# Performance work log

Hardware: AMD Instinct MI355X
Metric: run time of the kernel (lower is better)

## Reference

```python
import jax, jax.numpy as jnp
import numpy as np

B, S, D = 32, 512, 1024  # batch, seq_len, input_dim == output_dim


def setup_inputs() -> dict:
    key = jax.random.key(0)
    ks = jax.random.split(key, 13)
    std = 0.05  # tf.random_normal_initializer default stddev
    w = lambda k, shp: (jax.random.normal(k, shp, dtype=jnp.float32) * std)
    inp = {"seq_input_vec": jax.random.normal(ks[0], (B, S, D), dtype=jnp.float32)}
    names = ["Ui", "Wi", "Uf", "Wf", "Uo", "Wo", "Ug", "Wg"]
    for i, n in enumerate(names):
        inp[n] = w(ks[1 + i], (D, D))
    for n in ["bi", "bf", "bo", "bg"]:
        inp[n] = jnp.zeros((D,), dtype=jnp.float32)
    return inp


def reference(seq_input_vec, Ui, Wi, bi, Uf, Wf, bf, Uo, Wo, bo, Ug, Wg, bg):
    # seq_input_vec: [B, S, D]. Fuse the 4 input projections into one GEMM
    # over the whole sequence (mathematically identical to per-step matmuls).
    U = jnp.concatenate([Ui, Uf, Uo, Ug], axis=1)          # [D, 4D]
    W = jnp.concatenate([Wi, Wf, Wo, Wg], axis=1)          # [D, 4D]
    b = jnp.concatenate([bi, bf, bo, bg], axis=0)          # [4D]
    x_proj = jnp.einsum('bsd,de->sbe', seq_input_vec, U) + b  # [S, B, 4D]

    d = seq_input_vec.shape[-1]
    h0 = jnp.zeros((seq_input_vec.shape[0], d), dtype=seq_input_vec.dtype)
    c0 = jnp.zeros_like(h0)

    def step(carry, xp):
        c_prev, h_prev = carry
        z = xp + h_prev @ W                                 # [B, 4D]
        zi, zf, zo, zg = jnp.split(z, 4, axis=-1)
        i_t = jax.nn.sigmoid(zi)
        f_t = jax.nn.sigmoid(zf)
        o_t = jax.nn.sigmoid(zo)
        g_t = jnp.tanh(zg)
        # NOTE: original (nonstandard) math applies sigmoid to the cell update
        c_t = jax.nn.sigmoid(f_t * c_prev + i_t * g_t)
        h_t = jnp.tanh(c_t) * o_t
        return (c_t, h_t), h_t

    _, hs = jax.lax.scan(step, (c0, h0), x_proj)            # hs: [S, B, D]
    return jnp.transpose(hs, (1, 0, 2))                     # [B, S, D]
```

## Files before the change

### kernel.cpp

```cpp
#include <hip/hip_runtime.h>

typedef unsigned int u32;
typedef unsigned short u16;
typedef unsigned long long u64;
typedef __attribute__((ext_vector_type(8))) short short8;
typedef __attribute__((ext_vector_type(4))) float f32x4;
typedef __attribute__((ext_vector_type(4))) u32 u32x4;
typedef __attribute__((ext_vector_type(2))) u32 u32x2;

#define SEQ 512
#define BATCH 32
#define DIM 1024
#define NB 128

#define OFF_XT    0ull
#define OFF_UBT   33554432ull
#define OFF_WG2   41943040ull
#define OFF_XPROJ 50331648ull
#define OFF_BIAS  184680448ull
#define OFF_SYNC  184696832ull

__device__ __forceinline__ float bf2f(u16 u) {
  union { u32 u; float f; } v; v.u = ((u32)u) << 16; return v.f;
}
__device__ __forceinline__ u16 f2bf(float f) {
  union { float f; u32 u; } v; v.f = f;
  u32 r = v.u + 0x7FFFu + ((v.u >> 16) & 1u);
  return (u16)(r >> 16);
}
__device__ __forceinline__ float tanh_fast(float x) {
  return 1.f - 2.f / (1.f + __expf(2.f * x));
}
__device__ __forceinline__ void gload_lds16(const u16* g, u16* l) {
  __builtin_amdgcn_global_load_lds(
      (const __attribute__((address_space(1))) u32*)g,
      (__attribute__((address_space(3))) u32*)l, 16, 0, 0);
}
__device__ __forceinline__ void gload_lds16_coh(const u16* g, u16* l) {
  __builtin_amdgcn_global_load_lds(
      (const __attribute__((address_space(1))) u32*)g,
      (__attribute__((address_space(3))) u32*)l, 16, 0, 17);
}

__global__ void k_init(float* biasc, u32* sync, const float* bi,
                       const float* bfv, const float* bo, const float* bg) {
  int i = blockIdx.x * 256 + threadIdx.x;
  if (i < 4096) {
    int g = i >> 10, c = i & 1023;
    const float* p = (g == 0) ? bi : (g == 1) ? bfv : (g == 2) ? bo : bg;
    biasc[i] = p[c];
  } else if (i < 8192) {
    sync[i - 4096] = 0u;
  }
}

__global__ void k_zero(u32x4* p) {
  p[blockIdx.x * 256 + threadIdx.x] = (u32x4){0u, 0u, 0u, 0u};
}

__global__ void k_prep_w(const float* Ui, const float* Wi, const float* Uf,
                         const float* Wf, const float* Uo, const float* Wo,
                         const float* Ug, const float* Wg, u16* Ubt, u16* Wg2) {
  __shared__ float tile[64][65];
  int bx = blockIdx.x;
  int mi = bx >> 8;
  int tt = bx & 255;
  int tr = tt >> 4, tc = tt & 15;
  const float* src;
  switch (mi) {
    case 0: src = Ui; break; case 1: src = Wi; break;
    case 2: src = Uf; break; case 3: src = Wf; break;
    case 4: src = Uo; break; case 5: src = Wo; break;
    case 6: src = Ug; break; default: src = Wg; break;
  }
  int g = mi >> 1;
  int d0 = tr * 64, c0 = tc * 64;
  int ty = threadIdx.x >> 6, tx = threadIdx.x & 63;
#pragma unroll
  for (int i = 0; i < 16; ++i) {
    int r = i * 4 + ty;
    tile[r][tx] = src[(size_t)(d0 + r) * 1024 + c0 + tx];
  }
  __syncthreads();
  if (mi & 1) {
#pragma unroll
    for (int i = 0; i < 16; ++i) {
      int cc = i * 4 + ty;
      int c_full = c0 + cc;
      int k = d0 + tx;
      int blk = c_full >> 3;
      int lane = (((k & 31) >> 3) << 4) + ((c_full & 3) << 2) + g;
      size_t idx = (size_t)blk * 32768 +
                   (size_t)(((k >> 5) * 2 + ((c_full & 7) >> 2)) * 64 + lane) * 8 +
                   (k & 7);
      Wg2[idx] = f2bf(tile[tx][cc]);
    }
  } else {
#pragma unroll
    for (int i = 0; i < 16; ++i) {
      int cc = i * 4 + ty;
      Ubt[(size_t)((g << 10) + c0 + cc) * 1024 + d0 + tx] = f2bf(tile[tx][cc]);
    }
  }
}

__global__ void k_prep_x(const float* __restrict__ X, u16* __restrict__ Xt) {
  int idx = blockIdx.x * 256 + threadIdx.x;
  int m = idx >> 8, d4 = (idx & 255) << 2;
  int s = m >> 5, b = m & 31;
  const float4* p = (const float4*)(X + (size_t)(b * SEQ + s) * DIM + d4);
  float4 v = *p;
  u16 o[4] = { f2bf(v.x), f2bf(v.y), f2bf(v.z), f2bf(v.w) };
  *(ushort4*)(Xt + (size_t)m * DIM + d4) = *(ushort4*)o;
}

__global__ __launch_bounds__(256) void k_gemm(const u16* __restrict__ Xt,
                                              const u16* __restrict__ Ubt,
                                              const float* __restrict__ biasc,
                                              u16* __restrict__ xp2) {
  __shared__ u16 As[128 * 32];
  __shared__ u16 Bs[128 * 32];
  int tid = threadIdx.x;
  int w = tid >> 6, l = tid & 63;
  int n0 = blockIdx.x * 128, m0 = blockIdx.y * 128;
  int wm = w >> 1, wn = w & 1;
  int lrow = l & 15, lq = l >> 4;
  f32x4 acc[4][4] = {};
  for (int kt = 0; kt < 32; ++kt) {
    int k0 = kt * 32;
    __syncthreads();
#pragma unroll
    for (int is = 0; is < 2; ++is) {
      int c = is * 256 + w * 64 + l;
      int row = c >> 2, kg = c & 3;
      gload_lds16(Xt + (size_t)(m0 + row) * 1024 + k0 + kg * 8, As + c * 8);
      gload_lds16(Ubt + (size_t)(n0 + row) * 1024 + k0 + kg * 8, Bs + c * 8);
    }
    __syncthreads();
    short8 af[4], bfr[4];
#pragma unroll
    for (int mt = 0; mt < 4; ++mt)
      af[mt] = *(const short8*)(As + (wm * 64 + mt * 16 + lrow) * 32 + lq * 8);
#pragma unroll
    for (int nt = 0; nt < 4; ++nt)
      bfr[nt] = *(const short8*)(Bs + (wn * 64 + nt * 16 + lrow) * 32 + lq * 8);
#pragma unroll
    for (int mt = 0; mt < 4; ++mt)
#pragma unroll
      for (int nt = 0; nt < 4; ++nt)
        acc[mt][nt] = __builtin_amdgcn_mfma_f32_16x16x32_bf16(
            af[mt], bfr[nt], acc[mt][nt], 0, 0, 0);
  }
#pragma unroll
  for (int nt = 0; nt < 4; ++nt) {
    int col = n0 + wn * 64 + nt * 16 + lrow;
    float bv = biasc[col];
    int g = col >> 10, d = col & 1023;
    int blkd = d >> 3;
    int slot = ((d & 7) >> 2) * 4 + g;
    int lpart = (d & 3) * 16;
#pragma unroll
    for (int mt = 0; mt < 4; ++mt) {
      int rbase = m0 + wm * 64 + mt * 16 + lq * 4;
#pragma unroll
      for (int r = 0; r < 4; ++r) {
        int row = rbase + r;
        int s = row >> 5, b = row & 31;
        xp2[(size_t)(s * 128 + blkd) * 1024 + (lpart + (b & 15)) * 16 +
            (b >> 4) * 8 + slot] = f2bf(acc[mt][nt][r] + bv);
      }
    }
  }
}

__global__ __launch_bounds__(256, 1) void k_rec(const u16* __restrict__ Wg2,
                                                const u16* __restrict__ xp2,
                                                u16* hX, const u16* __restrict__ h0,
                                                u32* sync) {
  __shared__ u16 Hs[32768];
  int tid = threadIdx.x;
  int w = tid >> 6, l = tid & 63;
  int mt = w >> 1, nt = w & 1;
  int blk = blockIdx.x;
  int q = l >> 4, b15 = l & 15;

  short8 wf[32];
#pragma unroll
  for (int kt = 0; kt < 32; ++kt)
    wf[kt] = *(const short8*)(Wg2 + (size_t)blk * 32768 + (kt * 2 + mt) * 512 +
                              l * 8);
  u32x2 xqc, xqn;
  {
    const u16* xp = xp2 + (size_t)blk * 1024 + l * 16 + nt * 8 + mt * 4;
    asm volatile("global_load_dwordx2 %0, %1, off" : "=v"(xqc) : "v"(xp));
  }
  asm volatile("s_waitcnt vmcnt(0)" ::: "memory");
  __builtin_amdgcn_sched_barrier(0);

  int hoff = (((blk >> 2) * 2 + nt) * 64 + (blk & 3) * 16 + b15) * 8 + mt * 4 + q;
  float c_reg = 0.f;

  for (int s = 0; s < SEQ; ++s) {
    {
      u32 tgt = (u32)s;
      int guard = 0;
      for (;;) {
        u32 a = __hip_atomic_load(sync + l * 32, __ATOMIC_RELAXED,
                                  __HIP_MEMORY_SCOPE_AGENT);
        u32 b = __hip_atomic_load(sync + (64 + l) * 32, __ATOMIC_RELAXED,
                                  __HIP_MEMORY_SCOPE_AGENT);
        if (a >= tgt && b >= tgt) break;
        __builtin_amdgcn_s_sleep(1);
        if (++guard > 1000000) break;
      }
    }
    asm volatile("" ::: "memory");
    __builtin_amdgcn_sched_barrier(0);

    const u16* hs = (s == 0) ? h0 : (hX + (size_t)(s - 1) * 32768);
#pragma unroll
    for (int it = 0; it < 16; ++it)
      gload_lds16_coh(hs + (it * 256 + tid) * 8, Hs + (it * 256 + tid) * 8);
    {
      int sp = (s + 1 < SEQ) ? s + 1 : s;
      const u16* xp = xp2 + ((size_t)sp * 128 + blk) * 1024 + l * 16 +
                      nt * 8 + mt * 4;
      asm volatile("global_load_dwordx2 %0, %1, off" : "=v"(xqn) : "v"(xp));
    }

    f32x4 a0 = {0.f, 0.f, 0.f, 0.f}, a1 = {0.f, 0.f, 0.f, 0.f};
    asm volatile("s_waitcnt vmcnt(9)" ::: "memory");
    __builtin_amdgcn_sched_barrier(0);
    __builtin_amdgcn_s_barrier();
    __builtin_amdgcn_sched_barrier(0);
#pragma unroll
    for (int kt = 0; kt < 16; kt += 2) {
      short8 b0 = *(const short8*)(Hs + (kt * 2 + nt) * 512 + l * 8);
      short8 b1 = *(const short8*)(Hs + ((kt + 1) * 2 + nt) * 512 + l * 8);
      a0 = __builtin_amdgcn_mfma_f32_16x16x32_bf16(wf[kt], b0, a0, 0, 0, 0);
      a1 = __builtin_amdgcn_mfma_f32_16x16x32_bf16(wf[kt + 1], b1, a1, 0, 0, 0);
    }
    asm volatile("s_waitcnt vmcnt(1)" ::: "memory");
    __builtin_amdgcn_sched_barrier(0);
    __builtin_amdgcn_s_barrier();
    __builtin_amdgcn_sched_barrier(0);
#pragma unroll
    for (int kt = 16; kt < 32; kt += 2) {
      short8 b0 = *(const short8*)(Hs + (kt * 2 + nt) * 512 + l * 8);
      short8 b1 = *(const short8*)(Hs + ((kt + 1) * 2 + nt) * 512 + l * 8);
      a0 = __builtin_amdgcn_mfma_f32_16x16x32_bf16(wf[kt], b0, a0, 0, 0, 0);
      a1 = __builtin_amdgcn_mfma_f32_16x16x32_bf16(wf[kt + 1], b1, a1, 0, 0, 0);
    }
    f32x4 z4 = a0 + a1;

    union { u32x2 v; u16 a[4]; } xq;
    xq.v = xqc;
    float zi = z4[0] + bf2f(xq.a[0]);
    float zf = z4[1] + bf2f(xq.a[1]);
    float zo = z4[2] + bf2f(xq.a[2]);
    float zg = z4[3] + bf2f(xq.a[3]);
    float ig = 1.f / (1.f + __expf(-zi));
    float fg = 1.f / (1.f + __expf(-zf));
    float og = 1.f / (1.f + __expf(-zo));
    float gg = tanh_fast(zg);
    c_reg = 1.f / (1.f + __expf(-(fg * c_reg + ig * gg)));
    float h = tanh_fast(c_reg) * og;

    __hip_atomic_store(hX + (size_t)s * 32768 + hoff, f2bf(h),
                       __ATOMIC_RELAXED, __HIP_MEMORY_SCOPE_AGENT);
    __syncthreads();
    if (tid == 0)
      __hip_atomic_store(sync + blk * 32, (u32)(s + 1), __ATOMIC_RELAXED,
                         __HIP_MEMORY_SCOPE_AGENT);
    xqc = xqn;
  }
}

__global__ void k_out(const u16* __restrict__ hx, float* __restrict__ out) {
  int t = blockIdx.x * 256 + threadIdx.x;
  int d0 = (t & 127) << 3;
  int rem = t >> 7;
  int s = rem & 511, b = rem >> 9;
  int kt = d0 >> 5, jg = (d0 & 31) >> 3, ct = b >> 4;
  const u16* src = hx + (size_t)s * 32768 +
                   (size_t)(((kt * 2 + ct) * 64 + jg * 16 + (b & 15)) * 8);
  ushort4 v0 = *(const ushort4*)src;
  ushort4 v1 = *(const ushort4*)(src + 4);
  float4 o0 = { bf2f(v0.x), bf2f(v0.y), bf2f(v0.z), bf2f(v0.w) };
  float4 o1 = { bf2f(v1.x), bf2f(v1.y), bf2f(v1.z), bf2f(v1.w) };
  float* dst = out + (size_t)(b * SEQ + s) * DIM + d0;
  *(float4*)dst = o0;
  *(float4*)(dst + 4) = o1;
}

extern "C" void kernel_launch(void* const* d_in, const int* in_sizes, int n_in,
                              void* d_out, int out_size, void* d_ws,
                              size_t ws_size, hipStream_t stream) {
  const float* X   = (const float*)d_in[0];
  const float* Ui  = (const float*)d_in[1];
  const float* Wi  = (const float*)d_in[2];
  const float* Uf  = (const float*)d_in[3];
  const float* Wf  = (const float*)d_in[4];
  const float* Uo  = (const float*)d_in[5];
  const float* Wo  = (const float*)d_in[6];
  const float* Ug  = (const float*)d_in[7];
  const float* Wg  = (const float*)d_in[8];
  const float* bi  = (const float*)d_in[9];
  const float* bfv = (const float*)d_in[10];
  const float* bo  = (const float*)d_in[11];
  const float* bg  = (const float*)d_in[12];
  char* ws = (char*)d_ws;
  u16* Xt      = (u16*)(ws + OFF_XT);
  u16* Ubt     = (u16*)(ws + OFF_UBT);
  u16* Wg2     = (u16*)(ws + OFF_WG2);
  u16* xp2     = (u16*)(ws + OFF_XPROJ);
  float* biasc = (float*)(ws + OFF_BIAS);
  u32* sync    = (u32*)(ws + OFF_SYNC);
  float* out   = (float*)d_out;

  k_init<<<32, 256, 0, stream>>>(biasc, sync, bi, bfv, bo, bg);
  k_prep_w<<<2048, 256, 0, stream>>>(Ui, Wi, Uf, Wf, Uo, Wo, Ug, Wg, Ubt, Wg2);
  k_prep_x<<<16384, 256, 0, stream>>>(X, Xt);
  k_gemm<<<dim3(32, 128), 256, 0, stream>>>(Xt, Ubt, biasc, xp2);
  k_zero<<<16, 256, 0, stream>>>((u32x4*)Ubt);
  k_rec<<<NB, 256, 0, stream>>>(Wg2, xp2, Xt, Ubt, sync);
  k_out<<<8192, 256, 0, stream>>>(Xt, out);
}
```

Baseline: 2.107 ms.

## Replace flag-barrier recurrence sync with step-tagged hidden-state words and fewer larger blocks

The recurrent kernel drops the separate per-block sync counters and spin-wait barrier. Each hidden value is now published as a 32-bit word carrying the step number in its upper half, in a double-buffered tag array. Consumers load these words directly into registers, check the tags, and re-poll only the stale chunks, so per-step synchronisation is fused into the data loads. The grid also changes from 128 blocks of 256 threads to 64 blocks of 512 threads, with the recurrent weights held in LDS instead of registers. This trades larger hidden-state traffic (32-bit instead of 16-bit) and extra tag checks for fewer round-trip latencies per timestep.

```diff
diff --git a/kernel.cpp b/kernel.cpp
--- a/kernel.cpp
+++ b/kernel.cpp
@@ -11,14 +11,13 @@
 #define SEQ 512
 #define BATCH 32
 #define DIM 1024
-#define NB 128
+#define NB 64
 
 #define OFF_XT    0ull
 #define OFF_UBT   33554432ull
 #define OFF_WG2   41943040ull
 #define OFF_XPROJ 50331648ull
 #define OFF_BIAS  184680448ull
-#define OFF_SYNC  184696832ull
 
 __device__ __forceinline__ float bf2f(u16 u) {
   union { u32 u; float f; } v; v.u = ((u32)u) << 16; return v.f;
@@ -36,21 +35,14 @@
       (const __attribute__((address_space(1))) u32*)g,
       (__attribute__((address_space(3))) u32*)l, 16, 0, 0);
 }
-__device__ __forceinline__ void gload_lds16_coh(const u16* g, u16* l) {
-  __builtin_amdgcn_global_load_lds(
-      (const __attribute__((address_space(1))) u32*)g,
-      (__attribute__((address_space(3))) u32*)l, 16, 0, 17);
-}
-
-__global__ void k_init(float* biasc, u32* sync, const float* bi,
-                       const float* bfv, const float* bo, const float* bg) {
+
+__global__ void k_init(float* biasc, const float* bi, const float* bfv,
+                       const float* bo, const float* bg) {
   int i = blockIdx.x * 256 + threadIdx.x;
   if (i < 4096) {
     int g = i >> 10, c = i & 1023;
     const float* p = (g == 0) ? bi : (g == 1) ? bfv : (g == 2) ? bo : bg;
     biasc[i] = p[c];
-  } else if (i < 8192) {
-    sync[i - 4096] = 0u;
   }
 }
 
@@ -86,13 +78,14 @@
 #pragma unroll
     for (int i = 0; i < 16; ++i) {
       int cc = i * 4 + ty;
-      int c_full = c0 + cc;
+      int d = c0 + cc;
       int k = d0 + tx;
-      int blk = c_full >> 3;
-      int lane = (((k & 31) >> 3) << 4) + ((c_full & 3) << 2) + g;
-      size_t idx = (size_t)blk * 32768 +
-                   (size_t)(((k >> 5) * 2 + ((c_full & 7) >> 2)) * 64 + lane) * 8 +
-                   (k & 7);
+      int blk = d >> 4;
+      int m = (d & 15) * 4 + g;
+      int mt_ = m >> 4;
+      int lane = (((k & 31) >> 3) << 4) + (m & 15);
+      size_t idx = (size_t)blk * 65536 +
+                   (size_t)((((k >> 5) * 4 + mt_) * 64 + lane)) * 8 + (k & 7);
       Wg2[idx] = f2bf(tile[tx][cc]);
     }
   } else {
@@ -173,83 +166,104 @@
   }
 }
 
-__global__ __launch_bounds__(256, 1) void k_rec(const u16* __restrict__ Wg2,
+__global__ __launch_bounds__(512, 2) void k_rec(const u16* __restrict__ Wg2,
                                                 const u16* __restrict__ xp2,
-                                                u16* hX, const u16* __restrict__ h0,
-                                                u32* sync) {
-  __shared__ u16 Hs[32768];
+                                                u32* tg, u16* hX) {
+  __shared__ u16 Ws[65536];
   int tid = threadIdx.x;
   int w = tid >> 6, l = tid & 63;
   int mt = w >> 1, nt = w & 1;
   int blk = blockIdx.x;
   int q = l >> 4, b15 = l & 15;
-
-  short8 wf[32];
-#pragma unroll
-  for (int kt = 0; kt < 32; ++kt)
-    wf[kt] = *(const short8*)(Wg2 + (size_t)blk * 32768 + (kt * 2 + mt) * 512 +
-                              l * 8);
+#pragma unroll
+  for (int it = 0; it < 16; ++it) {
+    int c = it * 512 + tid;
+    gload_lds16(Wg2 + (size_t)blk * 65536 + c * 8, Ws + c * 8);
+  }
+  int dd = blk * 16 + mt * 4 + q;
+  int toff = (((dd >> 5) * 2 + nt) * 64 + (((dd & 31) >> 3) << 4) + b15) * 8 +
+             (dd & 7);
+  size_t xbase = ((size_t)(blk * 2 + (mt >> 1))) * 1024 +
+                 (q * 16 + b15) * 16 + nt * 8 + (mt & 1) * 4;
   u32x2 xqc, xqn;
-  {
-    const u16* xp = xp2 + (size_t)blk * 1024 + l * 16 + nt * 8 + mt * 4;
-    asm volatile("global_load_dwordx2 %0, %1, off" : "=v"(xqc) : "v"(xp));
-  }
+  asm volatile("global_load_dwordx2 %0, %1, off" : "=v"(xqc)
+               : "v"(xp2 + xbase));
   asm volatile("s_waitcnt vmcnt(0)" ::: "memory");
   __builtin_amdgcn_sched_barrier(0);
-
-  int hoff = (((blk >> 2) * 2 + nt) * 64 + (blk & 3) * 16 + b15) * 8 + mt * 4 + q;
   float c_reg = 0.f;
+  __syncthreads();
+
+  u32x4 qb[3][8];
+#define ISSUE(CB, C)                                                        \
+  _Pragma("unroll")                                                         \
+  for (int t4 = 0; t4 < 4; ++t4) {                                          \
+    const u32* bp = tgr + (((C) * 4 + t4) * 2 + nt) * 512 + l * 8;          \
+    asm volatile("global_load_dwordx4 %0, %1, off sc0 sc1"                  \
+                 : "=v"(qb[CB][t4 * 2]) : "v"(bp));                         \
+    asm volatile("global_load_dwordx4 %0, %1, off offset:16 sc0 sc1"        \
+                 : "=v"(qb[CB][t4 * 2 + 1]) : "v"(bp));                     \
+  }
 
   for (int s = 0; s < SEQ; ++s) {
-    {
-      u32 tgt = (u32)s;
-      int guard = 0;
-      for (;;) {
-        u32 a = __hip_atomic_load(sync + l * 32, __ATOMIC_RELAXED,
-                                  __HIP_MEMORY_SCOPE_AGENT);
-        u32 b = __hip_atomic_load(sync + (64 + l) * 32, __ATOMIC_RELAXED,
-                                  __HIP_MEMORY_SCOPE_AGENT);
-        if (a >= tgt && b >= tgt) break;
-        __builtin_amdgcn_s_sleep(1);
-        if (++guard > 1000000) break;
+    const u32* tgr = tg + (size_t)(s & 1) * 32768;
+    u32 T = (u32)s << 16;
+    ISSUE(0, 0) ISSUE(1, 1) ISSUE(2, 2)
+    f32x4 a0 = {0.f, 0.f, 0.f, 0.f}, a1 = {0.f, 0.f, 0.f, 0.f};
+#pragma unroll
+    for (int c = 0; c < 8; ++c) {
+      const int cb = c % 3;
+      if (c <= 5)      asm volatile("s_waitcnt vmcnt(16)" ::: "memory");
+      else if (c == 6) asm volatile("s_waitcnt vmcnt(8)" ::: "memory");
+      else             asm volatile("s_waitcnt vmcnt(0)" ::: "memory");
+      __builtin_amdgcn_sched_barrier(0);
+      u32 stale = 0u;
+#pragma unroll
+      for (int j = 0; j < 8; ++j) {
+        u32x4 v = qb[cb][j];
+        u32 m = ((v.x ^ T) | (v.y ^ T) | (v.z ^ T) | (v.w ^ T)) & 0xFFFF0000u;
+        stale |= m ? (1u << j) : 0u;
       }
-    }
-    asm volatile("" ::: "memory");
-    __builtin_amdgcn_sched_barrier(0);
-
-    const u16* hs = (s == 0) ? h0 : (hX + (size_t)(s - 1) * 32768);
-#pragma unroll
-    for (int it = 0; it < 16; ++it)
-      gload_lds16_coh(hs + (it * 256 + tid) * 8, Hs + (it * 256 + tid) * 8);
-    {
-      int sp = (s + 1 < SEQ) ? s + 1 : s;
-      const u16* xp = xp2 + ((size_t)sp * 128 + blk) * 1024 + l * 16 +
-                      nt * 8 + mt * 4;
-      asm volatile("global_load_dwordx2 %0, %1, off" : "=v"(xqn) : "v"(xp));
-    }
-
-    f32x4 a0 = {0.f, 0.f, 0.f, 0.f}, a1 = {0.f, 0.f, 0.f, 0.f};
-    asm volatile("s_waitcnt vmcnt(9)" ::: "memory");
-    __builtin_amdgcn_sched_barrier(0);
-    __builtin_amdgcn_s_barrier();
-    __builtin_amdgcn_sched_barrier(0);
-#pragma unroll
-    for (int kt = 0; kt < 16; kt += 2) {
-      short8 b0 = *(const short8*)(Hs + (kt * 2 + nt) * 512 + l * 8);
-      short8 b1 = *(const short8*)(Hs + ((kt + 1) * 2 + nt) * 512 + l * 8);
-      a0 = __builtin_amdgcn_mfma_f32_16x16x32_bf16(wf[kt], b0, a0, 0, 0, 0);
-      a1 = __builtin_amdgcn_mfma_f32_16x16x32_bf16(wf[kt + 1], b1, a1, 0, 0, 0);
-    }
-    asm volatile("s_waitcnt vmcnt(1)" ::: "memory");
-    __builtin_amdgcn_sched_barrier(0);
-    __builtin_amdgcn_s_barrier();
-    __builtin_amdgcn_sched_barrier(0);
-#pragma unroll
-    for (int kt = 16; kt < 32; kt += 2) {
-      short8 b0 = *(const short8*)(Hs + (kt * 2 + nt) * 512 + l * 8);
-      short8 b1 = *(const short8*)(Hs + ((kt + 1) * 2 + nt) * 512 + l * 8);
-      a0 = __builtin_amdgcn_mfma_f32_16x16x32_bf16(wf[kt], b0, a0, 0, 0, 0);
-      a1 = __builtin_amdgcn_mfma_f32_16x16x32_bf16(wf[kt + 1], b1, a1, 0, 0, 0);
+      if (__any((int)(stale != 0u))) {
+        int guard = 0;
+        do {
+          if (++guard > 1000000) break;
+          __builtin_amdgcn_s_sleep(2);
+#pragma unroll
+          for (int j = 0; j < 8; ++j)
+            if (stale & (1u << j)) {
+              const u32* bp = tgr + ((c * 4 + (j >> 1)) * 2 + nt) * 512 + l * 8 +
+                              (j & 1) * 4;
+              asm volatile("global_load_dwordx4 %0, %1, off sc0 sc1"
+                           : "=v"(qb[cb][j]) : "v"(bp));
+            }
+          asm volatile("s_waitcnt vmcnt(0)" ::: "memory");
+          __builtin_amdgcn_sched_barrier(0);
+          stale = 0u;
+#pragma unroll
+          for (int j = 0; j < 8; ++j) {
+            u32x4 v = qb[cb][j];
+            u32 m = ((v.x ^ T) | (v.y ^ T) | (v.z ^ T) | (v.w ^ T)) &
+                    0xFFFF0000u;
+            stale |= m ? (1u << j) : 0u;
+          }
+        } while (__any((int)(stale != 0u)));
+      }
+#pragma unroll
+      for (int t4 = 0; t4 < 4; ++t4) {
+        int kt = c * 4 + t4;
+        u32x4 A = qb[cb][t4 * 2], B = qb[cb][t4 * 2 + 1];
+        u32x4 pk = { __builtin_amdgcn_perm(A.y, A.x, 0x05040100u),
+                     __builtin_amdgcn_perm(A.w, A.z, 0x05040100u),
+                     __builtin_amdgcn_perm(B.y, B.x, 0x05040100u),
+                     __builtin_amdgcn_perm(B.w, B.z, 0x05040100u) };
+        short8 bfr = __builtin_bit_cast(short8, pk);
+        short8 wfr = *(const short8*)(Ws + (kt * 4 + mt) * 512 + l * 8);
+        if (kt & 1)
+          a1 = __builtin_amdgcn_mfma_f32_16x16x32_bf16(wfr, bfr, a1, 0, 0, 0);
+        else
+          a0 = __builtin_amdgcn_mfma_f32_16x16x32_bf16(wfr, bfr, a0, 0, 0, 0);
+      }
+      if (c <= 4) { ISSUE(cb, c + 3) }
     }
     f32x4 z4 = a0 + a1;
 
@@ -265,15 +279,20 @@
     float gg = tanh_fast(zg);
     c_reg = 1.f / (1.f + __expf(-(fg * c_reg + ig * gg)));
     float h = tanh_fast(c_reg) * og;
-
-    __hip_atomic_store(hX + (size_t)s * 32768 + hoff, f2bf(h),
+    u16 hb = f2bf(h);
+
+    __hip_atomic_store(tg + (size_t)((s + 1) & 1) * 32768 + toff,
+                       ((u32)(s + 1) << 16) | (u32)hb,
                        __ATOMIC_RELAXED, __HIP_MEMORY_SCOPE_AGENT);
-    __syncthreads();
-    if (tid == 0)
-      __hip_atomic_store(sync + blk * 32, (u32)(s + 1), __ATOMIC_RELAXED,
-                         __HIP_MEMORY_SCOPE_AGENT);
+    __builtin_nontemporal_store(hb, hX + (size_t)s * 32768 + toff);
+    {
+      int sp = (s + 1 < SEQ) ? s + 1 : s;
+      asm volatile("global_load_dwordx2 %0, %1, off" : "=v"(xqn)
+                   : "v"(xp2 + (size_t)sp * 131072 + xbase));
+    }
     xqc = xqn;
   }
+#undef ISSUE
 }
 
 __global__ void k_out(const u16* __restrict__ hx, float* __restrict__ out) {
@@ -311,18 +330,19 @@
   const float* bg  = (const float*)d_in[12];
   char* ws = (char*)d_ws;
   u16* Xt      = (u16*)(ws + OFF_XT);
+  u16* hX      = (u16*)(ws + OFF_XT);
   u16* Ubt     = (u16*)(ws + OFF_UBT);
+  u32* tg      = (u32*)(ws + OFF_UBT);
   u16* Wg2     = (u16*)(ws + OFF_WG2);
   u16* xp2     = (u16*)(ws + OFF_XPROJ);
   float* biasc = (float*)(ws + OFF_BIAS);
-  u32* sync    = (u32*)(ws + OFF_SYNC);
   float* out   = (float*)d_out;
 
-  k_init<<<32, 256, 0, stream>>>(biasc, sync, bi, bfv, bo, bg);
+  k_init<<<16, 256, 0, stream>>>(biasc, bi, bfv, bo, bg);
   k_prep_w<<<2048, 256, 0, stream>>>(Ui, Wi, Uf, Wf, Uo, Wo, Ug, Wg, Ubt, Wg2);
   k_prep_x<<<16384, 256, 0, stream>>>(X, Xt);
   k_gemm<<<dim3(32, 128), 256, 0, stream>>>(Xt, Ubt, biasc, xp2);
-  k_zero<<<16, 256, 0, stream>>>((u32x4*)Ubt);
-  k_rec<<<NB, 256, 0, stream>>>(Wg2, xp2, Xt, Ubt, sync);
-  k_out<<<8192, 256, 0, stream>>>(Xt, out);
-}
+  k_zero<<<64, 256, 0, stream>>>((u32x4*)tg);
+  k_rec<<<NB, 512, 0, stream>>>(Wg2, xp2, tg, hX);
+  k_out<<<8192, 256, 0, stream>>>(hX, out);
+}
```

Result: slower. 6.523 ms (+209.5%).

## Stage GEMM epilogue through LDS and prefetch x-projection into LDS double buffer

Applied to the files above, without the earlier changes.

The GEMM epilogue now writes its bf16 results into a shared-memory tile and then stores them to the xp2 layout with 16-byte coalesced writes, replacing scattered 2-byte stores. The recurrent kernel changes its x-projection layout to gate-major blocks and prefetches each step's slice into a double-buffered LDS array via async global-to-LDS loads, issued after the sync flag store. The goal is to remove uncoalesced writes and take the per-thread x-projection load out of the critical step. In exchange it adds LDS use, a full vmcnt(0) wait before the second MFMA half, and a dependence on the new layout matching in both kernels.

```diff
diff --git a/kernel.cpp b/kernel.cpp
--- a/kernel.cpp
+++ b/kernel.cpp
@@ -6,7 +6,6 @@
 typedef __attribute__((ext_vector_type(8))) short short8;
 typedef __attribute__((ext_vector_type(4))) float f32x4;
 typedef __attribute__((ext_vector_type(4))) u32 u32x4;
-typedef __attribute__((ext_vector_type(2))) u32 u32x2;
 
 #define SEQ 512
 #define BATCH 32
@@ -120,6 +119,7 @@
                                               u16* __restrict__ xp2) {
   __shared__ u16 As[128 * 32];
   __shared__ u16 Bs[128 * 32];
+  __shared__ u16 cbuf[4][16][8][32];
   int tid = threadIdx.x;
   int w = tid >> 6, l = tid & 63;
   int n0 = blockIdx.x * 128, m0 = blockIdx.y * 128;
@@ -153,23 +153,27 @@
   }
 #pragma unroll
   for (int nt = 0; nt < 4; ++nt) {
-    int col = n0 + wn * 64 + nt * 16 + lrow;
-    float bv = biasc[col];
-    int g = col >> 10, d = col & 1023;
-    int blkd = d >> 3;
-    int slot = ((d & 7) >> 2) * 4 + g;
-    int lpart = (d & 3) * 16;
+    int lc = wn * 64 + nt * 16 + lrow;
+    float bv = biasc[n0 + lc];
 #pragma unroll
     for (int mt = 0; mt < 4; ++mt) {
-      int rbase = m0 + wm * 64 + mt * 16 + lq * 4;
 #pragma unroll
       for (int r = 0; r < 4; ++r) {
-        int row = rbase + r;
-        int s = row >> 5, b = row & 31;
-        xp2[(size_t)(s * 128 + blkd) * 1024 + (lpart + (b & 15)) * 16 +
-            (b >> 4) * 8 + slot] = f2bf(acc[mt][nt][r] + bv);
+        int lr = wm * 64 + mt * 16 + lq * 4 + r;
+        cbuf[lr >> 5][lc >> 3][lrow & 7][lr & 31] = f2bf(acc[mt][nt][r] + bv);
       }
     }
+  }
+  __syncthreads();
+  int s0 = m0 >> 5, blkd0 = (n0 & 1023) >> 3, gb = (n0 >> 10) * 256;
+  const u16* cb = &cbuf[0][0][0][0];
+#pragma unroll
+  for (int i = 0; i < 8; ++i) {
+    int u = i * 256 + tid;
+    int r_ = u >> 5, w_ = u & 31;
+    u32x4 v = *(const u32x4*)(cb + u * 8);
+    *(u32x4*)(xp2 + (size_t)((s0 + (r_ >> 4)) * 128 + blkd0 + (r_ & 15)) * 1024 +
+              gb + w_ * 8) = v;
   }
 }
 
@@ -178,6 +182,7 @@
                                                 u16* hX, const u16* __restrict__ h0,
                                                 u32* sync) {
   __shared__ u16 Hs[32768];
+  __shared__ u16 XPs[2][1024];
   int tid = threadIdx.x;
   int w = tid >> 6, l = tid & 63;
   int mt = w >> 1, nt = w & 1;
@@ -189,16 +194,15 @@
   for (int kt = 0; kt < 32; ++kt)
     wf[kt] = *(const short8*)(Wg2 + (size_t)blk * 32768 + (kt * 2 + mt) * 512 +
                               l * 8);
-  u32x2 xqc, xqn;
-  {
-    const u16* xp = xp2 + (size_t)blk * 1024 + l * 16 + nt * 8 + mt * 4;
-    asm volatile("global_load_dwordx2 %0, %1, off" : "=v"(xqc) : "v"(xp));
-  }
+  if (tid < 128)
+    gload_lds16(xp2 + (size_t)blk * 1024 + tid * 8, XPs[0] + tid * 8);
   asm volatile("s_waitcnt vmcnt(0)" ::: "memory");
   __builtin_amdgcn_sched_barrier(0);
 
   int hoff = (((blk >> 2) * 2 + nt) * 64 + (blk & 3) * 16 + b15) * 8 + mt * 4 + q;
+  int xoff = (mt * 4 + q) * 32 + nt * 16 + b15;
   float c_reg = 0.f;
+  __syncthreads();
 
   for (int s = 0; s < SEQ; ++s) {
     {
@@ -221,15 +225,9 @@
 #pragma unroll
     for (int it = 0; it < 16; ++it)
       gload_lds16_coh(hs + (it * 256 + tid) * 8, Hs + (it * 256 + tid) * 8);
-    {
-      int sp = (s + 1 < SEQ) ? s + 1 : s;
-      const u16* xp = xp2 + ((size_t)sp * 128 + blk) * 1024 + l * 16 +
-                      nt * 8 + mt * 4;
-      asm volatile("global_load_dwordx2 %0, %1, off" : "=v"(xqn) : "v"(xp));
-    }
 
     f32x4 a0 = {0.f, 0.f, 0.f, 0.f}, a1 = {0.f, 0.f, 0.f, 0.f};
-    asm volatile("s_waitcnt vmcnt(9)" ::: "memory");
+    asm volatile("s_waitcnt vmcnt(8)" ::: "memory");
     __builtin_amdgcn_sched_barrier(0);
     __builtin_amdgcn_s_barrier();
     __builtin_amdgcn_sched_barrier(0);
@@ -240,7 +238,7 @@
       a0 = __builtin_amdgcn_mfma_f32_16x16x32_bf16(wf[kt], b0, a0, 0, 0, 0);
       a1 = __builtin_amdgcn_mfma_f32_16x16x32_bf16(wf[kt + 1], b1, a1, 0, 0, 0);
     }
-    asm volatile("s_waitcnt vmcnt(1)" ::: "memory");
+    asm volatile("s_waitcnt vmcnt(0)" ::: "memory");
     __builtin_amdgcn_sched_barrier(0);
     __builtin_amdgcn_s_barrier();
     __builtin_amdgcn_sched_barrier(0);
@@ -253,12 +251,11 @@
     }
     f32x4 z4 = a0 + a1;
 
-    union { u32x2 v; u16 a[4]; } xq;
-    xq.v = xqc;
-    float zi = z4[0] + bf2f(xq.a[0]);
-    float zf = z4[1] + bf2f(xq.a[1]);
-    float zo = z4[2] + bf2f(xq.a[2]);
-    float zg = z4[3] + bf2f(xq.a[3]);
+    const u16* xp = XPs[s & 1];
+    float zi = z4[0] + bf2f(xp[xoff]);
+    float zf = z4[1] + bf2f(xp[256 + xoff]);
+    float zo = z4[2] + bf2f(xp[512 + xoff]);
+    float zg = z4[3] + bf2f(xp[768 + xoff]);
     float ig = 1.f / (1.f + __expf(-zi));
     float fg = 1.f / (1.f + __expf(-zf));
     float og = 1.f / (1.f + __expf(-zo));
@@ -272,7 +269,12 @@
     if (tid == 0)
       __hip_atomic_store(sync + blk * 32, (u32)(s + 1), __ATOMIC_RELAXED,
                          __HIP_MEMORY_SCOPE_AGENT);
-    xqc = xqn;
+    {
+      int sp = (s + 1 < SEQ) ? s + 1 : s;
+      if (tid < 128)
+        gload_lds16(xp2 + ((size_t)sp * 128 + blk) * 1024 + tid * 8,
+                    XPs[(s + 1) & 1] + tid * 8);
+    }
   }
 }
 
```

Measured after the change: 1.789 ms. 15.1% less time.
